# Kernel optimization log

Measured on AMD Instinct MI355X. Metric: run time of the kernel, lower is better.

Reference implementation:

```python
import jax, jax.numpy as jnp
import numpy as np

N = 100000        # nodes
E = 1600000       # edges (N * avg_degree 16)
D_IN = 128
D_OUT = 32
OBS_T = 60        # observation_time -> decay table size 60*OBS_T = 3600
T_MAX = 60 * OBS_T


def setup_inputs() -> dict:
    key = jax.random.key(0)
    ks = jax.random.split(key, 8)
    inp = {
        "input": jax.random.normal(ks[0], (N, D_IN), dtype=jnp.float32),
        "W": jax.random.normal(ks[1], (D_IN, D_OUT), dtype=jnp.float32) * (np.sqrt(2.0) / np.sqrt(D_IN)),
        # decay weights are abs(normal(0, 0.02)) in the original; rand*0.04 is same scale
        "decay_weight1": jnp.abs(jax.random.normal(ks[2], (T_MAX, 1), dtype=jnp.float32) * 0.02),
        "decay_weight2": jnp.abs(jax.random.normal(ks[3], (T_MAX, 1), dtype=jnp.float32) * 0.02),
        "edge_row": jax.random.randint(ks[4], (E,), 0, N, dtype=jnp.int32),
        "edge_col": jax.random.randint(ks[5], (E,), 0, N, dtype=jnp.int32),
        # zero-based interval index; equals (adj_value - 1) of the original code
        "edge_time": jax.random.randint(ks[6], (E,), 0, T_MAX, dtype=jnp.int32),
        "arrive_time": jax.random.randint(ks[7], (N,), 0, T_MAX, dtype=jnp.int32),
        "observation_time": OBS_T,
    }
    return inp


def reference(input, W, decay_weight1, decay_weight2,
              edge_row, edge_col, edge_time, arrive_time, observation_time):
    n_nodes = input.shape[0]
    # h = relu(input @ W)  [N, D_OUT]
    h = jax.nn.relu(jnp.matmul(input, W))
    # one-hot(interval) @ decay_weight1 == embedding lookup  -> per-edge decay scalar
    decay = decay_weight1[edge_time, 0]                        # [E]
    # SpecialSpmm: out[i] = sum_{edges (i,j)} decay_e * h[j]  (gather-scale-scatter)
    msgs = decay[:, None] * h[edge_col]                        # [E, D_OUT]
    h_prime = jax.ops.segment_sum(msgs, edge_row, num_segments=n_nodes)
    # outlayer window decay: one-hot(60*T - arrive - 1) @ decay_weight2 == lookup
    win_idx = 60 * observation_time - arrive_time - 1          # [N] in [0, 60*T)
    h_prime = decay_weight2[win_idx, 0][:, None] * h_prime
    return h_prime
```

## Files before the change

### kernel.cpp

```cpp
#include <hip/hip_runtime.h>

#define N_NODES 100000
#define N_EDGES 1600000
#define D_IN    128
#define D_OUT   32
#define CROWS   2048
#define NCB     49
#define NSH     8
#define CAP_A   4500
#define DEPTH   48
#define NROWP   (NCB * CROWS)
#define CAP_R   64
#define GEMM_BLKS ((N_NODES + 63) / 64)
#define GRID_A  2048
#define EPB_A   ((N_EDGES + GRID_A - 1) / GRID_A)
#define RPB3    32
#define K3_BLKS (N_NODES / RPB3)

typedef __attribute__((ext_vector_type(8))) short bf16x8;
typedef __attribute__((ext_vector_type(4))) float f32x4;

__device__ inline short f2bf(float f) {
    union { float f; unsigned u; } v; v.f = f;
    unsigned r = (v.u + 0x7FFFu + ((v.u >> 16) & 1u)) >> 16;
    return (short)r;
}

union SMemGA {
    struct { short wbt[D_IN * D_OUT]; } g;
    struct { uint2 lbin[NCB][DEPTH]; int lcnt[NCB]; int gbase[NCB]; } a;
};

__global__ __launch_bounds__(256) void gemm_phaseA_kernel(
    const float* __restrict__ input, const float* __restrict__ W,
    const int* __restrict__ erow,    const int* __restrict__ ecol,
    const int* __restrict__ etime,
    unsigned short* __restrict__ h16,
    int* __restrict__ gcur,
    uint2* __restrict__ segA)
{
    __shared__ SMemGA sm;
    const int tid = threadIdx.x;

    if (blockIdx.x < GEMM_BLKS) {
        for (int i = tid; i < D_IN * D_OUT; i += 256) {
            const int k = i >> 5, c = i & 31;
            sm.g.wbt[c * D_IN + k] = f2bf(W[i]);
        }
        __syncthreads();

        const int wave = tid >> 6;
        const int lane = tid & 63;
        const int r0   = blockIdx.x * 64 + wave * 16;
        const int c16  = lane & 15;
        const int quad = lane >> 4;

        int ra = r0 + c16;
        if (ra >= N_NODES) ra = N_NODES - 1;
        const float* arow = input + (size_t)ra * D_IN;

        f32x4 acc0 = {0.f, 0.f, 0.f, 0.f};
        f32x4 acc1 = {0.f, 0.f, 0.f, 0.f};
#pragma unroll
        for (int q = 0; q < 4; ++q) {
            const float* ap = arow + q * 32 + quad * 8;
            f32x4 a0 = *(const f32x4*)(ap);
            f32x4 a1 = *(const f32x4*)(ap + 4);
            bf16x8 af;
            af[0] = f2bf(a0.x); af[1] = f2bf(a0.y); af[2] = f2bf(a0.z); af[3] = f2bf(a0.w);
            af[4] = f2bf(a1.x); af[5] = f2bf(a1.y); af[6] = f2bf(a1.z); af[7] = f2bf(a1.w);
            bf16x8 b0 = *(const bf16x8*)(sm.g.wbt + (c16)      * D_IN + q * 32 + quad * 8);
            bf16x8 b1 = *(const bf16x8*)(sm.g.wbt + (c16 + 16) * D_IN + q * 32 + quad * 8);
            acc0 = __builtin_amdgcn_mfma_f32_16x16x32_bf16(af, b0, acc0, 0, 0, 0);
            acc1 = __builtin_amdgcn_mfma_f32_16x16x32_bf16(af, b1, acc1, 0, 0, 0);
        }
#pragma unroll
        for (int i = 0; i < 4; ++i) {
            const int rr = r0 + quad * 4 + i;
            if (rr < N_NODES) {
                h16[(size_t)rr * D_OUT + c16]      = (unsigned short)f2bf(fmaxf(acc0[i], 0.f));
                h16[(size_t)rr * D_OUT + c16 + 16] = (unsigned short)f2bf(fmaxf(acc1[i], 0.f));
            }
        }
    } else {
        const int blk   = blockIdx.x - GEMM_BLKS;
        const int shard = blk & (NSH - 1);
        const int wv    = tid >> 6;
        const int ln    = tid & 63;

        if (tid < NCB) sm.a.lcnt[tid] = 0;
        __syncthreads();

        const int e_beg = blk * EPB_A;
        const int e_end = min(e_beg + EPB_A, N_EDGES);

        for (int e = e_beg + tid; e < e_end; e += 256) {
            const int row = erow[e];
            const int cb  = row >> 11;
            uint2 p;
            p.x = (unsigned)ecol[e] | ((unsigned)(row & (CROWS - 1)) << 17);
            p.y = (unsigned)etime[e];
            const int pos = atomicAdd(&sm.a.lcnt[cb], 1);
            if (pos < DEPTH) sm.a.lbin[cb][pos] = p;
            else {
                const int gp = atomicAdd(&gcur[(cb * NSH + shard) * 16], 1);
                if (gp < CAP_A) segA[(size_t)(cb * NSH + shard) * CAP_A + gp] = p;
            }
        }
        __syncthreads();

        if (tid < NCB) {
            const int c = min(sm.a.lcnt[tid], DEPTH);
            sm.a.gbase[tid] = atomicAdd(&gcur[(tid * NSH + shard) * 16], c);
        }
        __syncthreads();

        for (int bin = wv; bin < NCB; bin += 4) {
            const int c  = min(sm.a.lcnt[bin], DEPTH);
            const int gb = sm.a.gbase[bin];
            uint2* seg = segA + (size_t)(bin * NSH + shard) * CAP_A;
            for (int k = ln; k < c; k += 64)
                if (gb + k < CAP_A) seg[gb + k] = sm.a.lbin[bin][k];
        }
    }
}

__global__ __launch_bounds__(256) void phaseB_kernel(
    const int* __restrict__ gcur, const uint2* __restrict__ segA,
    int* __restrict__ fcur,
    unsigned* __restrict__ spk2)
{
    __shared__ int hist[CROWS];
    __shared__ int curs[CROWS];

    const int tid    = threadIdx.x;
    const int seg_id = blockIdx.x >> 1;
    const int half   = blockIdx.x & 1;
    const int cb     = seg_id >> 3;
    const int shard  = seg_id & 7;
    const int ntot   = min(gcur[(cb * NSH + shard) * 16], CAP_A);
    const int nh     = (ntot + 1) >> 1;
    const int beg    = half * nh;
    const int end    = min(ntot, beg + nh);
    const uint2* seg = segA + (size_t)(cb * NSH + shard) * CAP_A;

    for (int t = tid; t < CROWS; t += 256) hist[t] = 0;
    __syncthreads();

    for (int i = beg + tid; i < end; i += 256)
        atomicAdd(&hist[(seg[i].x >> 17) & (CROWS - 1)], 1);
    __syncthreads();

    for (int t = tid; t < CROWS; t += 256) {
        const int h = hist[t];
        curs[t] = h ? atomicAdd(&fcur[cb * CROWS + t], h) : 0;
    }
    __syncthreads();

    for (int i = beg + tid; i < end; i += 256) {
        const uint2 p   = seg[i];
        const int   fl  = (p.x >> 17) & (CROWS - 1);
        const unsigned rec = (p.x & 0x1FFFFu) | (p.y << 20);
        const int pos = atomicAdd(&curs[fl], 1);
        if (pos < CAP_R)
            spk2[((size_t)(cb * CROWS + fl) << 6) + pos] = rec;
    }
}

__global__ __launch_bounds__(256) void row_reduce_kernel(
    const unsigned short* __restrict__ h16, const int* __restrict__ fcur,
    const unsigned* __restrict__ spk2, const float* __restrict__ dw1,
    const float* __restrict__ dw2, const int* __restrict__ arrive,
    const int* __restrict__ obs, float* __restrict__ out)
{
    __shared__ unsigned pk[RPB3][CAP_R + 4];
    __shared__ int ncnt[RPB3];

    const int tid = threadIdx.x;
    const int b   = blockIdx.x;

    const uint4* src = (const uint4*)(spk2 + ((size_t)b * RPB3 << 6));
#pragma unroll
    for (int i = 0; i < 2; ++i) {
        const int idx = tid + i * 256;
        const uint4 v = src[idx];
        *(uint4*)&pk[idx >> 4][(idx & 15) * 4] = v;
    }
    if (tid < RPB3) ncnt[tid] = min(fcur[b * RPB3 + tid], CAP_R);
    __syncthreads();

    const int g  = tid >> 3;
    const int li = tid & 7;
    const int r  = b * RPB3 + g;
    const int n  = ncnt[g];
    const unsigned short* hp = h16 + li * 4;

    float a0 = 0.f, a1 = 0.f, a2 = 0.f, a3 = 0.f;
    int j = 0;
    for (; j + 8 <= n; j += 8) {
#pragma unroll
        for (int u = 0; u < 8; ++u) {
            const unsigned rec = pk[g][j + u];
            const uint2 hv = *(const uint2*)(hp + ((size_t)(rec & 0x1FFFFu) << 5));
            const float w  = dw1[rec >> 20];
            a0 = fmaf(w, __uint_as_float(hv.x << 16),         a0);
            a1 = fmaf(w, __uint_as_float(hv.x & 0xFFFF0000u), a1);
            a2 = fmaf(w, __uint_as_float(hv.y << 16),         a2);
            a3 = fmaf(w, __uint_as_float(hv.y & 0xFFFF0000u), a3);
        }
    }
    for (; j < n; ++j) {
        const unsigned rec = pk[g][j];
        const uint2 hv = *(const uint2*)(hp + ((size_t)(rec & 0x1FFFFu) << 5));
        const float w  = dw1[rec >> 20];
        a0 = fmaf(w, __uint_as_float(hv.x << 16),         a0);
        a1 = fmaf(w, __uint_as_float(hv.x & 0xFFFF0000u), a1);
        a2 = fmaf(w, __uint_as_float(hv.y << 16),         a2);
        a3 = fmaf(w, __uint_as_float(hv.y & 0xFFFF0000u), a3);
    }

    const int T = 60 * obs[0];
    const float sdw = dw2[T - arrive[r] - 1];
    float4 o;
    o.x = a0 * sdw; o.y = a1 * sdw; o.z = a2 * sdw; o.w = a3 * sdw;
    *(float4*)(out + ((size_t)r << 5) + li * 4) = o;
}

extern "C" void kernel_launch(void* const* d_in, const int* in_sizes, int n_in,
                              void* d_out, int out_size, void* d_ws, size_t ws_size,
                              hipStream_t stream)
{
    const float* input  = (const float*)d_in[0];
    const float* W      = (const float*)d_in[1];
    const float* dw1    = (const float*)d_in[2];
    const float* dw2    = (const float*)d_in[3];
    const int*   erow   = (const int*)d_in[4];
    const int*   ecol   = (const int*)d_in[5];
    const int*   etime  = (const int*)d_in[6];
    const int*   arrive = (const int*)d_in[7];
    const int*   obs    = (const int*)d_in[8];

    float* out = (float*)d_out;

    char* p = (char*)d_ws;
    unsigned short* h16 = (unsigned short*)p;
    p += (size_t)N_NODES * D_OUT * 2;
    p = (char*)(((size_t)p + 255) & ~(size_t)255);
    int* gcur = (int*)p;
    p += (size_t)NCB * NSH * 16 * 4;
    int* fcur = (int*)p;
    p += (size_t)NROWP * 4;
    p = (char*)(((size_t)p + 255) & ~(size_t)255);
    uint2* segA = (uint2*)p;
    p += (size_t)NCB * NSH * CAP_A * 8;
    p = (char*)(((size_t)p + 255) & ~(size_t)255);
    unsigned* spk2 = (unsigned*)p;
    p += (size_t)NROWP * CAP_R * 4;

    hipMemsetAsync(gcur, 0, (size_t)(NCB * NSH * 16 + NROWP) * 4, stream);

    gemm_phaseA_kernel<<<GEMM_BLKS + GRID_A, 256, 0, stream>>>(
        input, W, erow, ecol, etime, h16, gcur, segA);
    phaseB_kernel<<<NCB * NSH * 2, 256, 0, stream>>>(gcur, segA, fcur, spk2);
    row_reduce_kernel<<<K3_BLKS, 256, 0, stream>>>(
        h16, fcur, spk2, dw1, dw2, arrive, obs, out);
}
```

Baseline: 189.3 us.

## Fuse row sort and reduction into one kernel with finer 256-row bins

Edges are now binned into 391 buckets of 256 rows instead of 49 buckets of 2048. The separate phase B scatter kernel and the padded 64-slot per-row buffer are gone. A single sort_reduce kernel per bucket builds a row histogram, runs a prefix scan, counting-sorts the records into shared memory and then reduces each row. This drops one launch, the fcur memset and a global round trip through spk2. The cost is only 391 blocks in the reduce phase with an in-block scan, plus tighter fixed capacities (CAP_S, CAP_B) that could silently drop edges on skewed inputs.

Result: slower. 212.5 us (+12.3%).

```diff
diff --git a/kernel.cpp b/kernel.cpp
--- a/kernel.cpp
+++ b/kernel.cpp
@@ -4,18 +4,15 @@
 #define N_EDGES 1600000
 #define D_IN    128
 #define D_OUT   32
-#define CROWS   2048
-#define NCB     49
+#define NBIN    391
+#define NBINP   392
 #define NSH     8
-#define CAP_A   4500
-#define DEPTH   48
-#define NROWP   (NCB * CROWS)
-#define CAP_R   64
+#define CAP_S   768
+#define DEPTH   10
+#define CAP_B   4736
 #define GEMM_BLKS ((N_NODES + 63) / 64)
-#define GRID_A  2048
+#define GRID_A  1024
 #define EPB_A   ((N_EDGES + GRID_A - 1) / GRID_A)
-#define RPB3    32
-#define K3_BLKS (N_NODES / RPB3)
 
 typedef __attribute__((ext_vector_type(8))) short bf16x8;
 typedef __attribute__((ext_vector_type(4))) float f32x4;
@@ -28,7 +25,7 @@
 
 union SMemGA {
     struct { short wbt[D_IN * D_OUT]; } g;
-    struct { uint2 lbin[NCB][DEPTH]; int lcnt[NCB]; int gbase[NCB]; } a;
+    struct { uint2 lbin[NBIN][DEPTH]; int lcnt[NBIN]; int gbase[NBIN]; } a;
 };
 
 __global__ __launch_bounds__(256) void gemm_phaseA_kernel(
@@ -88,7 +85,7 @@
         const int wv    = tid >> 6;
         const int ln    = tid & 63;
 
-        if (tid < NCB) sm.a.lcnt[tid] = 0;
+        for (int t = tid; t < NBIN; t += 256) sm.a.lcnt[t] = 0;
         __syncthreads();
 
         const int e_beg = blk * EPB_A;
@@ -96,111 +93,116 @@
 
         for (int e = e_beg + tid; e < e_end; e += 256) {
             const int row = erow[e];
-            const int cb  = row >> 11;
+            const int bn  = row >> 8;
             uint2 p;
-            p.x = (unsigned)ecol[e] | ((unsigned)(row & (CROWS - 1)) << 17);
+            p.x = (unsigned)ecol[e] | ((unsigned)(row & 255) << 17);
             p.y = (unsigned)etime[e];
-            const int pos = atomicAdd(&sm.a.lcnt[cb], 1);
-            if (pos < DEPTH) sm.a.lbin[cb][pos] = p;
+            const int pos = atomicAdd(&sm.a.lcnt[bn], 1);
+            if (pos < DEPTH) sm.a.lbin[bn][pos] = p;
             else {
-                const int gp = atomicAdd(&gcur[(cb * NSH + shard) * 16], 1);
-                if (gp < CAP_A) segA[(size_t)(cb * NSH + shard) * CAP_A + gp] = p;
+                const int gp = atomicAdd(&gcur[(bn * NSH + shard) * 4], 1);
+                if (gp < CAP_S) segA[(size_t)(bn * NSH + shard) * CAP_S + gp] = p;
             }
         }
         __syncthreads();
 
-        if (tid < NCB) {
-            const int c = min(sm.a.lcnt[tid], DEPTH);
-            sm.a.gbase[tid] = atomicAdd(&gcur[(tid * NSH + shard) * 16], c);
-        }
-        __syncthreads();
-
-        for (int bin = wv; bin < NCB; bin += 4) {
-            const int c  = min(sm.a.lcnt[bin], DEPTH);
-            const int gb = sm.a.gbase[bin];
-            uint2* seg = segA + (size_t)(bin * NSH + shard) * CAP_A;
+        for (int t = tid; t < NBIN; t += 256) {
+            const int c = min(sm.a.lcnt[t], DEPTH);
+            sm.a.gbase[t] = atomicAdd(&gcur[(t * NSH + shard) * 4], c);
+        }
+        __syncthreads();
+
+        for (int bn = wv; bn < NBIN; bn += 4) {
+            const int c  = min(sm.a.lcnt[bn], DEPTH);
+            const int gb = sm.a.gbase[bn];
+            uint2* seg = segA + (size_t)(bn * NSH + shard) * CAP_S;
             for (int k = ln; k < c; k += 64)
-                if (gb + k < CAP_A) seg[gb + k] = sm.a.lbin[bin][k];
-        }
-    }
-}
-
-__global__ __launch_bounds__(256) void phaseB_kernel(
-    const int* __restrict__ gcur, const uint2* __restrict__ segA,
-    int* __restrict__ fcur,
-    unsigned* __restrict__ spk2)
-{
-    __shared__ int hist[CROWS];
-    __shared__ int curs[CROWS];
-
-    const int tid    = threadIdx.x;
-    const int seg_id = blockIdx.x >> 1;
-    const int half   = blockIdx.x & 1;
-    const int cb     = seg_id >> 3;
-    const int shard  = seg_id & 7;
-    const int ntot   = min(gcur[(cb * NSH + shard) * 16], CAP_A);
-    const int nh     = (ntot + 1) >> 1;
-    const int beg    = half * nh;
-    const int end    = min(ntot, beg + nh);
-    const uint2* seg = segA + (size_t)(cb * NSH + shard) * CAP_A;
-
-    for (int t = tid; t < CROWS; t += 256) hist[t] = 0;
-    __syncthreads();
-
-    for (int i = beg + tid; i < end; i += 256)
-        atomicAdd(&hist[(seg[i].x >> 17) & (CROWS - 1)], 1);
-    __syncthreads();
-
-    for (int t = tid; t < CROWS; t += 256) {
-        const int h = hist[t];
-        curs[t] = h ? atomicAdd(&fcur[cb * CROWS + t], h) : 0;
-    }
-    __syncthreads();
-
-    for (int i = beg + tid; i < end; i += 256) {
-        const uint2 p   = seg[i];
-        const int   fl  = (p.x >> 17) & (CROWS - 1);
-        const unsigned rec = (p.x & 0x1FFFFu) | (p.y << 20);
-        const int pos = atomicAdd(&curs[fl], 1);
-        if (pos < CAP_R)
-            spk2[((size_t)(cb * CROWS + fl) << 6) + pos] = rec;
-    }
-}
-
-__global__ __launch_bounds__(256) void row_reduce_kernel(
-    const unsigned short* __restrict__ h16, const int* __restrict__ fcur,
-    const unsigned* __restrict__ spk2, const float* __restrict__ dw1,
+                if (gb + k < CAP_S) seg[gb + k] = sm.a.lbin[bn][k];
+        }
+    }
+}
+
+__global__ __launch_bounds__(256) void sort_reduce_kernel(
+    const unsigned short* __restrict__ h16, const int* __restrict__ gcur,
+    const uint2* __restrict__ segA, const float* __restrict__ dw1,
     const float* __restrict__ dw2, const int* __restrict__ arrive,
     const int* __restrict__ obs, float* __restrict__ out)
 {
-    __shared__ unsigned pk[RPB3][CAP_R + 4];
-    __shared__ int ncnt[RPB3];
+    __shared__ int hist[256];
+    __shared__ int scan[256];
+    __shared__ int start[256];
+    __shared__ int curs[256];
+    __shared__ unsigned dense[CAP_B];
 
     const int tid = threadIdx.x;
     const int b   = blockIdx.x;
 
-    const uint4* src = (const uint4*)(spk2 + ((size_t)b * RPB3 << 6));
-#pragma unroll
-    for (int i = 0; i < 2; ++i) {
-        const int idx = tid + i * 256;
-        const uint4 v = src[idx];
-        *(uint4*)&pk[idx >> 4][(idx & 15) * 4] = v;
-    }
-    if (tid < RPB3) ncnt[tid] = min(fcur[b * RPB3 + tid], CAP_R);
+    hist[tid] = 0;
+    __syncthreads();
+
+#pragma unroll
+    for (int s = 0; s < NSH; ++s) {
+        const int n = min(gcur[(b * NSH + s) * 4], CAP_S);
+        const uint2* seg = segA + (size_t)(b * NSH + s) * CAP_S;
+        for (int i = tid; i < n; i += 256)
+            atomicAdd(&hist[(seg[i].x >> 17) & 255], 1);
+    }
+    __syncthreads();
+
+    scan[tid] = hist[tid];
+    __syncthreads();
+    for (int off = 1; off < 256; off <<= 1) {
+        int v = scan[tid];
+        if (tid >= off) v += scan[tid - off];
+        __syncthreads();
+        scan[tid] = v;
+        __syncthreads();
+    }
+    start[tid] = scan[tid] - hist[tid];
+    curs[tid]  = scan[tid] - hist[tid];
+    __syncthreads();
+
+#pragma unroll
+    for (int s = 0; s < NSH; ++s) {
+        const int n = min(gcur[(b * NSH + s) * 4], CAP_S);
+        const uint2* seg = segA + (size_t)(b * NSH + s) * CAP_S;
+        for (int i = tid; i < n; i += 256) {
+            const uint2 p  = seg[i];
+            const int   rl = (p.x >> 17) & 255;
+            const unsigned rec = (p.x & 0x1FFFFu) | (p.y << 20);
+            const int pos = atomicAdd(&curs[rl], 1);
+            if (pos < CAP_B) dense[pos] = rec;
+        }
+    }
     __syncthreads();
 
     const int g  = tid >> 3;
     const int li = tid & 7;
-    const int r  = b * RPB3 + g;
-    const int n  = ncnt[g];
+    const int T  = 60 * obs[0];
     const unsigned short* hp = h16 + li * 4;
 
-    float a0 = 0.f, a1 = 0.f, a2 = 0.f, a3 = 0.f;
-    int j = 0;
-    for (; j + 8 <= n; j += 8) {
-#pragma unroll
-        for (int u = 0; u < 8; ++u) {
-            const unsigned rec = pk[g][j + u];
+    for (int rsub = g; rsub < 256; rsub += 32) {
+        const int row = b * 256 + rsub;
+        if (row >= N_NODES) break;
+        const int beg = start[rsub];
+        const int end = min(beg + hist[rsub], CAP_B);
+
+        float a0 = 0.f, a1 = 0.f, a2 = 0.f, a3 = 0.f;
+        int j = beg;
+        for (; j + 8 <= end; j += 8) {
+#pragma unroll
+            for (int u = 0; u < 8; ++u) {
+                const unsigned rec = dense[j + u];
+                const uint2 hv = *(const uint2*)(hp + ((size_t)(rec & 0x1FFFFu) << 5));
+                const float w  = dw1[rec >> 20];
+                a0 = fmaf(w, __uint_as_float(hv.x << 16),         a0);
+                a1 = fmaf(w, __uint_as_float(hv.x & 0xFFFF0000u), a1);
+                a2 = fmaf(w, __uint_as_float(hv.y << 16),         a2);
+                a3 = fmaf(w, __uint_as_float(hv.y & 0xFFFF0000u), a3);
+            }
+        }
+        for (; j < end; ++j) {
+            const unsigned rec = dense[j];
             const uint2 hv = *(const uint2*)(hp + ((size_t)(rec & 0x1FFFFu) << 5));
             const float w  = dw1[rec >> 20];
             a0 = fmaf(w, __uint_as_float(hv.x << 16),         a0);
@@ -208,22 +210,12 @@
             a2 = fmaf(w, __uint_as_float(hv.y << 16),         a2);
             a3 = fmaf(w, __uint_as_float(hv.y & 0xFFFF0000u), a3);
         }
-    }
-    for (; j < n; ++j) {
-        const unsigned rec = pk[g][j];
-        const uint2 hv = *(const uint2*)(hp + ((size_t)(rec & 0x1FFFFu) << 5));
-        const float w  = dw1[rec >> 20];
-        a0 = fmaf(w, __uint_as_float(hv.x << 16),         a0);
-        a1 = fmaf(w, __uint_as_float(hv.x & 0xFFFF0000u), a1);
-        a2 = fmaf(w, __uint_as_float(hv.y << 16),         a2);
-        a3 = fmaf(w, __uint_as_float(hv.y & 0xFFFF0000u), a3);
-    }
-
-    const int T = 60 * obs[0];
-    const float sdw = dw2[T - arrive[r] - 1];
-    float4 o;
-    o.x = a0 * sdw; o.y = a1 * sdw; o.z = a2 * sdw; o.w = a3 * sdw;
-    *(float4*)(out + ((size_t)r << 5) + li * 4) = o;
+
+        const float sdw = dw2[T - arrive[row] - 1];
+        float4 o;
+        o.x = a0 * sdw; o.y = a1 * sdw; o.z = a2 * sdw; o.w = a3 * sdw;
+        *(float4*)(out + ((size_t)row << 5) + li * 4) = o;
+    }
 }
 
 extern "C" void kernel_launch(void* const* d_in, const int* in_sizes, int n_in,
@@ -247,21 +239,14 @@
     p += (size_t)N_NODES * D_OUT * 2;
     p = (char*)(((size_t)p + 255) & ~(size_t)255);
     int* gcur = (int*)p;
-    p += (size_t)NCB * NSH * 16 * 4;
-    int* fcur = (int*)p;
-    p += (size_t)NROWP * 4;
+    p += (size_t)NBINP * NSH * 4 * 4;
     p = (char*)(((size_t)p + 255) & ~(size_t)255);
     uint2* segA = (uint2*)p;
-    p += (size_t)NCB * NSH * CAP_A * 8;
-    p = (char*)(((size_t)p + 255) & ~(size_t)255);
-    unsigned* spk2 = (unsigned*)p;
-    p += (size_t)NROWP * CAP_R * 4;
-
-    hipMemsetAsync(gcur, 0, (size_t)(NCB * NSH * 16 + NROWP) * 4, stream);
+
+    hipMemsetAsync(gcur, 0, (size_t)NBINP * NSH * 4 * 4, stream);
 
     gemm_phaseA_kernel<<<GEMM_BLKS + GRID_A, 256, 0, stream>>>(
         input, W, erow, ecol, etime, h16, gcur, segA);
-    phaseB_kernel<<<NCB * NSH * 2, 256, 0, stream>>>(gcur, segA, fcur, spk2);
-    row_reduce_kernel<<<K3_BLKS, 256, 0, stream>>>(
-        h16, fcur, spk2, dw1, dw2, arrive, obs, out);
-}
+    sort_reduce_kernel<<<NBIN, 256, 0, stream>>>(
+        h16, gcur, segA, dw1, dw2, arrive, obs, out);
+}
```

## Replace fixed-capacity row slots with per-column-block counting sort into CSR

Applied to the files above, without the earlier changes.

The second phase now runs one 512-thread block per 2048-row column block. Each block builds a histogram over all shards, prefix-scans it, and scatters records into a compact CSR-like layout with per-row start offsets, replacing the fixed 64-slot-per-row buckets and their global atomics. The reduce kernel stages a contiguous span of records per 32-row group into shared memory, falling back to global loads when the span overflows. This shrinks the scatter buffer, removes the per-row cap that could drop edges, and drops most of the memset. In exchange, phase two has only 49 blocks, which limits parallelism.

Result: slower. 203.2 us (+7.4%).

```diff
diff --git a/kernel.cpp b/kernel.cpp
--- a/kernel.cpp
+++ b/kernel.cpp
@@ -10,12 +10,13 @@
 #define CAP_A   4500
 #define DEPTH   48
 #define NROWP   (NCB * CROWS)
-#define CAP_R   64
+#define CBCAP   36864
+#define CAPW    768
+#define RPB3    32
+#define K3_BLKS (NCB * 64)
 #define GEMM_BLKS ((N_NODES + 63) / 64)
 #define GRID_A  2048
 #define EPB_A   ((N_EDGES + GRID_A - 1) / GRID_A)
-#define RPB3    32
-#define K3_BLKS (N_NODES / RPB3)
 
 typedef __attribute__((ext_vector_type(8))) short bf16x8;
 typedef __attribute__((ext_vector_type(4))) float f32x4;
@@ -125,74 +126,103 @@
     }
 }
 
-__global__ __launch_bounds__(256) void phaseB_kernel(
+__global__ __launch_bounds__(512) void sortcb_kernel(
     const int* __restrict__ gcur, const uint2* __restrict__ segA,
-    int* __restrict__ fcur,
+    int* __restrict__ rstart, int* __restrict__ fcur,
     unsigned* __restrict__ spk2)
 {
     __shared__ int hist[CROWS];
+    __shared__ int sstart[CROWS];
     __shared__ int curs[CROWS];
-
-    const int tid    = threadIdx.x;
-    const int seg_id = blockIdx.x >> 1;
-    const int half   = blockIdx.x & 1;
-    const int cb     = seg_id >> 3;
-    const int shard  = seg_id & 7;
-    const int ntot   = min(gcur[(cb * NSH + shard) * 16], CAP_A);
-    const int nh     = (ntot + 1) >> 1;
-    const int beg    = half * nh;
-    const int end    = min(ntot, beg + nh);
-    const uint2* seg = segA + (size_t)(cb * NSH + shard) * CAP_A;
-
-    for (int t = tid; t < CROWS; t += 256) hist[t] = 0;
-    __syncthreads();
-
-    for (int i = beg + tid; i < end; i += 256)
-        atomicAdd(&hist[(seg[i].x >> 17) & (CROWS - 1)], 1);
-    __syncthreads();
-
-    for (int t = tid; t < CROWS; t += 256) {
-        const int h = hist[t];
-        curs[t] = h ? atomicAdd(&fcur[cb * CROWS + t], h) : 0;
-    }
-    __syncthreads();
-
-    for (int i = beg + tid; i < end; i += 256) {
-        const uint2 p   = seg[i];
-        const int   fl  = (p.x >> 17) & (CROWS - 1);
-        const unsigned rec = (p.x & 0x1FFFFu) | (p.y << 20);
-        const int pos = atomicAdd(&curs[fl], 1);
-        if (pos < CAP_R)
-            spk2[((size_t)(cb * CROWS + fl) << 6) + pos] = rec;
+    __shared__ int part[512];
+    __shared__ int snsh[NSH];
+
+    const int tid = threadIdx.x;
+    const int cb  = blockIdx.x;
+
+    if (tid < NSH) snsh[tid] = min(gcur[(cb * NSH + tid) * 16], CAP_A);
+    for (int t = tid; t < CROWS; t += 512) hist[t] = 0;
+    __syncthreads();
+
+    for (int s = 0; s < NSH; ++s) {
+        const int n = snsh[s];
+        const uint2* seg = segA + (size_t)(cb * NSH + s) * CAP_A;
+        for (int i = tid; i < n; i += 512)
+            atomicAdd(&hist[(seg[i].x >> 17) & (CROWS - 1)], 1);
+    }
+    __syncthreads();
+
+    int tmp[4]; int s0 = 0;
+    const int base = tid * 4;
+#pragma unroll
+    for (int k = 0; k < 4; ++k) { tmp[k] = hist[base + k]; s0 += tmp[k]; }
+    part[tid] = s0;
+    __syncthreads();
+    for (int off = 1; off < 512; off <<= 1) {
+        int v = part[tid];
+        if (tid >= off) v += part[tid - off];
+        __syncthreads(); part[tid] = v; __syncthreads();
+    }
+    int run = part[tid] - s0;
+#pragma unroll
+    for (int k = 0; k < 4; ++k) { sstart[base + k] = run; curs[base + k] = run; run += tmp[k]; }
+    __syncthreads();
+
+    for (int t = tid; t < CROWS; t += 512) {
+        rstart[cb * CROWS + t] = cb * CBCAP + sstart[t];
+        fcur[cb * CROWS + t]   = hist[t];
+    }
+
+    unsigned* dst = spk2 + (size_t)cb * CBCAP;
+    for (int s = 0; s < NSH; ++s) {
+        const int n = snsh[s];
+        const uint2* seg = segA + (size_t)(cb * NSH + s) * CAP_A;
+        for (int i = tid; i < n; i += 512) {
+            const uint2 p  = seg[i];
+            const int   rl = (p.x >> 17) & (CROWS - 1);
+            const unsigned rec = (p.x & 0x1FFFFu) | (p.y << 20);
+            dst[atomicAdd(&curs[rl], 1)] = rec;
+        }
     }
 }
 
 __global__ __launch_bounds__(256) void row_reduce_kernel(
-    const unsigned short* __restrict__ h16, const int* __restrict__ fcur,
-    const unsigned* __restrict__ spk2, const float* __restrict__ dw1,
-    const float* __restrict__ dw2, const int* __restrict__ arrive,
-    const int* __restrict__ obs, float* __restrict__ out)
-{
-    __shared__ unsigned pk[RPB3][CAP_R + 4];
-    __shared__ int ncnt[RPB3];
-
+    const unsigned short* __restrict__ h16, const int* __restrict__ rstart,
+    const int* __restrict__ fcur, const unsigned* __restrict__ spk2,
+    const float* __restrict__ dw1, const float* __restrict__ dw2,
+    const int* __restrict__ arrive, const int* __restrict__ obs,
+    float* __restrict__ out)
+{
+    __shared__ unsigned st[CAPW];
+    __shared__ int ls[RPB3];
+    __shared__ int lc[RPB3];
+
+    const int b  = blockIdx.x;
+    const int cb = b >> 6;
+    const int r0 = cb * CROWS + (b & 63) * RPB3;
+    if (r0 >= N_NODES) return;
     const int tid = threadIdx.x;
-    const int b   = blockIdx.x;
-
-    const uint4* src = (const uint4*)(spk2 + ((size_t)b * RPB3 << 6));
-#pragma unroll
-    for (int i = 0; i < 2; ++i) {
-        const int idx = tid + i * 256;
-        const uint4 v = src[idx];
-        *(uint4*)&pk[idx >> 4][(idx & 15) * 4] = v;
-    }
-    if (tid < RPB3) ncnt[tid] = min(fcur[b * RPB3 + tid], CAP_R);
+
+    if (tid < RPB3) {
+        ls[tid] = rstart[r0 + tid];
+        lc[tid] = fcur[r0 + tid];
+    }
+    __syncthreads();
+
+    const int sbeg  = ls[0];
+    const int span  = ls[RPB3 - 1] + lc[RPB3 - 1] - sbeg;
+    const int spanc = min(span, CAPW);
+    for (int i = tid; i < spanc; i += 256) st[i] = spk2[(size_t)sbeg + i];
     __syncthreads();
 
     const int g  = tid >> 3;
     const int li = tid & 7;
-    const int r  = b * RPB3 + g;
-    const int n  = ncnt[g];
+    const int row = r0 + g;
+    const int beg = ls[g] - sbeg;
+    const int n   = lc[g];
+    const unsigned* recs = (beg + n <= CAPW)
+        ? (const unsigned*)&st[beg]
+        : (const unsigned*)&spk2[(size_t)sbeg + beg];
     const unsigned short* hp = h16 + li * 4;
 
     float a0 = 0.f, a1 = 0.f, a2 = 0.f, a3 = 0.f;
@@ -200,7 +230,7 @@
     for (; j + 8 <= n; j += 8) {
 #pragma unroll
         for (int u = 0; u < 8; ++u) {
-            const unsigned rec = pk[g][j + u];
+            const unsigned rec = recs[j + u];
             const uint2 hv = *(const uint2*)(hp + ((size_t)(rec & 0x1FFFFu) << 5));
             const float w  = dw1[rec >> 20];
             a0 = fmaf(w, __uint_as_float(hv.x << 16),         a0);
@@ -210,7 +240,7 @@
         }
     }
     for (; j < n; ++j) {
-        const unsigned rec = pk[g][j];
+        const unsigned rec = recs[j];
         const uint2 hv = *(const uint2*)(hp + ((size_t)(rec & 0x1FFFFu) << 5));
         const float w  = dw1[rec >> 20];
         a0 = fmaf(w, __uint_as_float(hv.x << 16),         a0);
@@ -220,10 +250,10 @@
     }
 
     const int T = 60 * obs[0];
-    const float sdw = dw2[T - arrive[r] - 1];
+    const float sdw = dw2[T - arrive[row] - 1];
     float4 o;
     o.x = a0 * sdw; o.y = a1 * sdw; o.z = a2 * sdw; o.w = a3 * sdw;
-    *(float4*)(out + ((size_t)r << 5) + li * 4) = o;
+    *(float4*)(out + ((size_t)row << 5) + li * 4) = o;
 }
 
 extern "C" void kernel_launch(void* const* d_in, const int* in_sizes, int n_in,
@@ -248,6 +278,8 @@
     p = (char*)(((size_t)p + 255) & ~(size_t)255);
     int* gcur = (int*)p;
     p += (size_t)NCB * NSH * 16 * 4;
+    int* rstart = (int*)p;
+    p += (size_t)NROWP * 4;
     int* fcur = (int*)p;
     p += (size_t)NROWP * 4;
     p = (char*)(((size_t)p + 255) & ~(size_t)255);
@@ -255,13 +287,12 @@
     p += (size_t)NCB * NSH * CAP_A * 8;
     p = (char*)(((size_t)p + 255) & ~(size_t)255);
     unsigned* spk2 = (unsigned*)p;
-    p += (size_t)NROWP * CAP_R * 4;
-
-    hipMemsetAsync(gcur, 0, (size_t)(NCB * NSH * 16 + NROWP) * 4, stream);
+
+    hipMemsetAsync(gcur, 0, (size_t)NCB * NSH * 16 * 4, stream);
 
     gemm_phaseA_kernel<<<GEMM_BLKS + GRID_A, 256, 0, stream>>>(
         input, W, erow, ecol, etime, h16, gcur, segA);
-    phaseB_kernel<<<NCB * NSH * 2, 256, 0, stream>>>(gcur, segA, fcur, spk2);
+    sortcb_kernel<<<NCB, 512, 0, stream>>>(gcur, segA, rstart, fcur, spk2);
     row_reduce_kernel<<<K3_BLKS, 256, 0, stream>>>(
-        h16, fcur, spk2, dw1, dw2, arrive, obs, out);
-}
+        h16, rstart, fcur, spk2, dw1, dw2, arrive, obs, out);
+}
```
